# Performance work log

Measured on AMD Instinct MI355X. Metric: run time of the kernel, lower is better.

Reference implementation:

```python
import jax, jax.numpy as jnp
import numpy as np

B, P, T = 128, 196, 20
VOCAB, ENC, EMB, DEC, ATTN = 10000, 2048, 512, 512, 512


def _linear_params(key, out_dim, in_dim):
    kw, kb = jax.random.split(key)
    s = 1.0 / np.sqrt(in_dim)
    W = jax.random.uniform(kw, (out_dim, in_dim), minval=-s, maxval=s, dtype=jnp.float32)
    b = jax.random.uniform(kb, (out_dim,), minval=-s, maxval=s, dtype=jnp.float32)
    return W, b


def setup_inputs() -> dict:
    key = jax.random.key(0)
    ks = jax.random.split(key, 12)
    enc_w, enc_b = _linear_params(ks[0], ATTN, ENC)
    dec_w, dec_b = _linear_params(ks[1], ATTN, DEC)
    full_w, full_b = _linear_params(ks[2], 1, ATTN)
    W_ih, b_ih = _linear_params(ks[3], 4 * DEC, EMB + ENC)
    W_hh, b_hh = _linear_params(ks[4], 4 * DEC, DEC)
    ih_w, ih_b = _linear_params(ks[5], DEC, ENC)
    ic_w, ic_b = _linear_params(ks[6], DEC, ENC)
    fc_w, fc_b = _linear_params(ks[7], VOCAB, DEC)
    return {
        "encoder_out": jax.random.normal(ks[8], (B, P, ENC), dtype=jnp.float32),
        "captions": jax.random.randint(ks[9], (B, T), 0, VOCAB, dtype=jnp.int32),
        "lengths": jax.random.randint(ks[10], (B,), 1, T + 1, dtype=jnp.int32),
        "embedding": jax.random.normal(ks[11], (VOCAB, EMB), dtype=jnp.float32),
        "enc_attn_w": enc_w, "enc_attn_b": enc_b,
        "dec_attn_w": dec_w, "dec_attn_b": dec_b,
        "full_attn_w": full_w, "full_attn_b": full_b,
        "W_ih": W_ih, "b_ih": b_ih, "W_hh": W_hh, "b_hh": b_hh,
        "init_h_w": ih_w, "init_h_b": ih_b,
        "init_c_w": ic_w, "init_c_b": ic_b,
        "fc_w": fc_w, "fc_b": fc_b,
    }


def reference(encoder_out, captions, lengths, embedding,
              enc_attn_w, enc_attn_b, dec_attn_w, dec_attn_b,
              full_attn_w, full_attn_b, W_ih, b_ih, W_hh, b_hh,
              init_h_w, init_h_b, init_c_w, init_c_b, fc_w, fc_b):
    # init hidden state from mean-pooled encoder features
    mean_enc = encoder_out.mean(axis=1)                      # [B, ENC]
    h = mean_enc @ init_h_w.T + init_h_b                      # [B, DEC]
    c = mean_enc @ init_c_w.T + init_c_b

    # loop-invariant encoder projection for additive attention
    attn_enc = jnp.einsum('bpe,ae->bpa', encoder_out, enc_attn_w) + enc_attn_b  # [B, P, ATTN]

    embs = embedding[captions]                                # [B, T, EMB]
    embs_t = jnp.swapaxes(embs, 0, 1)                         # [T, B, EMB]

    dec = h.shape[1]

    def step(carry, emb_t):
        h, c = carry
        # additive attention
        attn_dec = h @ dec_attn_w.T + dec_attn_b              # [B, ATTN]
        energy = jnp.einsum('bpa,a->bp', jax.nn.relu(attn_enc + attn_dec[:, None, :]), full_attn_w[0]) + full_attn_b[0]
        alpha = jax.nn.softmax(energy, axis=1)                # [B, P]
        context = jnp.einsum('bpe,bp->be', encoder_out, alpha)  # [B, ENC]
        # LSTMCell
        x = jnp.concatenate([emb_t, context], axis=1)
        gates = x @ W_ih.T + b_ih + h @ W_hh.T + b_hh          # [B, 4*DEC]
        i, f, g, o = jnp.split(gates, 4, axis=1)
        c_new = jax.nn.sigmoid(f) * c + jax.nn.sigmoid(i) * jnp.tanh(g)
        h_new = jax.nn.sigmoid(o) * jnp.tanh(c_new)
        preds = h_new @ fc_w.T + fc_b                          # [B, VOCAB] (dropout in eval mode = identity)
        return (h_new, c_new), (preds, alpha)

    (_, _), (outputs_t, alphas_t) = jax.lax.scan(step, (h, c), embs_t)
    outputs = jnp.swapaxes(outputs_t, 0, 1)                   # [B, T, VOCAB]
    alphas = jnp.swapaxes(alphas_t, 0, 1)                     # [B, T, P]
    return outputs, alphas
```

## Files before the change

### kernel.cpp

```cpp
#include <hip/hip_runtime.h>

constexpr int kB = 128, kP = 196, kT = 20;
constexpr int kVocab = 10000, kEnc = 2048, kEmb = 512, kDec = 512, kAttn = 512;

typedef __bf16 b16x8 __attribute__((ext_vector_type(8)));
typedef __bf16 b16x4 __attribute__((ext_vector_type(4)));
typedef float f32x4 __attribute__((ext_vector_type(4)));
typedef unsigned short u16x4 __attribute__((ext_vector_type(4)));

__device__ __forceinline__ unsigned short f2bf(float f) {
  unsigned int u = __float_as_uint(f);
  u += 0x7fffu + ((u >> 16) & 1u);
  return (unsigned short)(u >> 16);
}
__device__ __forceinline__ float bf2f(unsigned short h) {
  return __uint_as_float(((unsigned int)h) << 16);
}

__device__ __forceinline__ void async16(const void* g, void* l) {
  __builtin_amdgcn_global_load_lds(
      (const __attribute__((address_space(1))) unsigned int*)g,
      (__attribute__((address_space(3))) unsigned int*)l, 16, 0, 0);
}

template <bool OUT_BF16>
__global__ __launch_bounds__(256) void gemm128(
    const unsigned short* __restrict__ A, const unsigned short* __restrict__ W,
    const float* __restrict__ bias, float* __restrict__ C,
    unsigned short* __restrict__ Cb, int M, int N, int K, long ldc) {
  __shared__ unsigned short sA[128 * 32];
  __shared__ unsigned short sB[128 * 32];
  const int tid = threadIdx.x;
  const int lane = tid & 63;
  const int wave = tid >> 6;
  const int wm = wave >> 1, wn = wave & 1;
  const int m0 = blockIdx.y * 128;
  const int n0 = blockIdx.x * 128;
  const int q = lane >> 4, l = lane & 15;

  const int srow = tid >> 2;
  const int skk = (tid & 3) * 8;
  f32x4 acc[4][4] = {};

  for (int k0 = 0; k0 < K; k0 += 32) {
#pragma unroll
    for (int g = 0; g < 2; g++) {
      const int r = g * 64 + srow;
      async16(A + (long)(m0 + r) * K + k0 + skk, &sA[r * 32 + skk]);
      async16(W + (long)(n0 + r) * K + k0 + skk, &sB[r * 32 + skk]);
    }
    __syncthreads();
    b16x8 af[4], bf[4];
#pragma unroll
    for (int i = 0; i < 4; i++) {
      af[i] = *(const b16x8*)&sA[(wm * 64 + 16 * i + l) * 32 + q * 8];
      bf[i] = *(const b16x8*)&sB[(wn * 64 + 16 * i + l) * 32 + q * 8];
    }
#pragma unroll
    for (int i = 0; i < 4; i++)
#pragma unroll
      for (int j = 0; j < 4; j++)
        acc[i][j] = __builtin_amdgcn_mfma_f32_16x16x32_bf16(af[i], bf[j], acc[i][j], 0, 0, 0);
    __syncthreads();
  }

#pragma unroll
  for (int i = 0; i < 4; i++)
#pragma unroll
    for (int j = 0; j < 4; j++) {
      const int col = n0 + wn * 64 + 16 * j + l;
      const float bv = bias ? bias[col] : 0.0f;
#pragma unroll
      for (int r = 0; r < 4; r++) {
        const int row = m0 + wm * 64 + 16 * i + q * 4 + r;
        const float v = acc[i][j][r] + bv;
        if (OUT_BF16) Cb[(long)row * ldc + col] = f2bf(v);
        else          C[(long)row * ldc + col] = v;
      }
    }
}

template <bool A_BF16, bool OUT_BF16>
__global__ __launch_bounds__(256) void gemm_bt(
    const void* __restrict__ A_, const unsigned short* __restrict__ W,
    const float* __restrict__ bias, float* __restrict__ C,
    unsigned short* __restrict__ Cb, int M, int N, int K, long ldc) {
  const int lane = threadIdx.x & 63;
  const int wave = threadIdx.x >> 6;
  const int wm = wave >> 1, wn = wave & 1;
  const int m0 = blockIdx.y * 64 + wm * 32;
  const int n0 = blockIdx.x * 64 + wn * 32;
  const int q = lane >> 4;
  const int l = lane & 15;
  f32x4 acc[2][2] = {};
  const unsigned short* Ab = (const unsigned short*)A_;
  const float* Af = (const float*)A_;

  for (int k0 = 0; k0 < K; k0 += 32) {
    const int ka = k0 + q * 8;
    b16x8 af[2], wf[2];
#pragma unroll
    for (int i = 0; i < 2; i++) {
      int r = m0 + 16 * i + l;
      if (r >= M) r = M - 1;
      if (A_BF16) {
        af[i] = *(const b16x8*)(Ab + (long)r * K + ka);
      } else {
        const float* p = Af + (long)r * K + ka;
        const f32x4 lo = *(const f32x4*)p;
        const f32x4 hi = *(const f32x4*)(p + 4);
        b16x8 t;
#pragma unroll
        for (int j = 0; j < 4; j++) {
          ((unsigned short*)&t)[j] = f2bf(lo[j]);
          ((unsigned short*)&t)[4 + j] = f2bf(hi[j]);
        }
        af[i] = t;
      }
    }
#pragma unroll
    for (int j = 0; j < 2; j++) {
      int r = n0 + 16 * j + l;
      if (r >= N) r = N - 1;
      wf[j] = *(const b16x8*)(W + (long)r * K + ka);
    }
#pragma unroll
    for (int i = 0; i < 2; i++)
#pragma unroll
      for (int j = 0; j < 2; j++)
        acc[i][j] = __builtin_amdgcn_mfma_f32_16x16x32_bf16(af[i], wf[j], acc[i][j], 0, 0, 0);
  }

#pragma unroll
  for (int i = 0; i < 2; i++)
#pragma unroll
    for (int j = 0; j < 2; j++) {
      const int col = n0 + 16 * j + l;
      if (col >= N) continue;
      const float bv = bias ? bias[col] : 0.0f;
#pragma unroll
      for (int r = 0; r < 4; r++) {
        const int row = m0 + 16 * i + q * 4 + r;
        if (row >= M) continue;
        const float v = acc[i][j][r] + bv;
        if (OUT_BF16) Cb[(long)row * ldc + col] = f2bf(v);
        else          C[(long)row * ldc + col] = v;
      }
    }
}

template <bool SRC_BF16>
__global__ __launch_bounds__(256) void attn_step(
    const void* __restrict__ enc_, const unsigned short* __restrict__ attn_enc_bf,
    const unsigned short* __restrict__ h_bf, const unsigned short* __restrict__ daw_bf,
    const float* __restrict__ dab, const float* __restrict__ faw, const float* __restrict__ fab,
    float* __restrict__ alphas, unsigned short* __restrict__ ctx, int t) {
  const int b = blockIdx.x;
  const int half = blockIdx.y;
  const int tid = threadIdx.x;
  const int lane = tid & 63, wave = tid >> 6;
  __shared__ float h_s[512];
  __shared__ float ad_s[512];
  __shared__ float e_sm[kP];
  __shared__ float red[4];

  h_s[tid] = bf2f(h_bf[b * kDec + tid]);
  h_s[tid + 256] = bf2f(h_bf[b * kDec + tid + 256]);
  __syncthreads();

#pragma unroll
  for (int cc = 0; cc < 2; cc++) {
    const int j = tid + cc * 256;
    float s = dab[j];
    const unsigned short* wrow = daw_bf + (long)j * kDec;
    for (int k = 0; k < kDec; k += 8) {
      const b16x8 wv = *(const b16x8*)(wrow + k);
#pragma unroll
      for (int jj = 0; jj < 8; jj++)
        s += bf2f(((const unsigned short*)&wv)[jj]) * h_s[k + jj];
    }
    ad_s[j] = s;
  }
  __syncthreads();

  float ad8[8], w8[8];
  const int a0 = lane * 8;
#pragma unroll
  for (int j = 0; j < 8; j++) { ad8[j] = ad_s[a0 + j]; w8[j] = faw[a0 + j]; }
  const float fb0 = fab[0];
  for (int p = wave; p < kP; p += 4) {
    const b16x8 rv = *(const b16x8*)(attn_enc_bf + ((long)(b * kP + p)) * kAttn + a0);
    float s = 0.f;
#pragma unroll
    for (int j = 0; j < 8; j++)
      s += w8[j] * fmaxf(bf2f(((const unsigned short*)&rv)[j]) + ad8[j], 0.f);
#pragma unroll
    for (int off = 32; off > 0; off >>= 1) s += __shfl_down(s, off, 64);
    if (lane == 0) e_sm[p] = s + fb0;
  }
  __syncthreads();

  const float v = (tid < kP) ? e_sm[tid] : -3.0e38f;
  float m = v;
#pragma unroll
  for (int off = 32; off > 0; off >>= 1) m = fmaxf(m, __shfl_down(m, off, 64));
  if (lane == 0) red[wave] = m;
  __syncthreads();
  m = fmaxf(fmaxf(red[0], red[1]), fmaxf(red[2], red[3]));
  const float ex = (tid < kP) ? expf(v - m) : 0.f;
  float s = ex;
#pragma unroll
  for (int off = 32; off > 0; off >>= 1) s += __shfl_down(s, off, 64);
  if (lane == 0) red[wave] = s;
  __syncthreads();
  s = red[0] + red[1] + red[2] + red[3];
  __syncthreads();
  const float alpha = ex / s;
  if (tid < kP) {
    e_sm[tid] = alpha;
    if (half == 0) alphas[((long)b * kT + t) * kP + tid] = alpha;
  }
  __syncthreads();

  const int e = half * 1024 + tid * 4;
  float a4[4] = {};
  if (SRC_BF16) {
    const unsigned short* base = (const unsigned short*)enc_ + (long)b * kP * kEnc + e;
    for (int p = 0; p < kP; p++) {
      const float a = e_sm[p];
      const b16x4 rv = *(const b16x4*)(base + (long)p * kEnc);
#pragma unroll
      for (int j = 0; j < 4; j++) a4[j] += a * bf2f(((const unsigned short*)&rv)[j]);
    }
  } else {
    const float* base = (const float*)enc_ + (long)b * kP * kEnc + e;
    for (int p = 0; p < kP; p++) {
      const float a = e_sm[p];
      const f32x4 rv = *(const f32x4*)(base + (long)p * kEnc);
#pragma unroll
      for (int j = 0; j < 4; j++) a4[j] += a * rv[j];
    }
  }
  u16x4 o;
#pragma unroll
  for (int j = 0; j < 4; j++) o[j] = f2bf(a4[j]);
  *(u16x4*)(ctx + (long)b * kEnc + e) = o;
}

__global__ __launch_bounds__(256) void gemm_gates(
    const unsigned short* __restrict__ embs_t, const unsigned short* __restrict__ ctx,
    const unsigned short* __restrict__ hbf, const unsigned short* __restrict__ Wih,
    const unsigned short* __restrict__ Whh, float* __restrict__ gates_part) {
  const int lane = threadIdx.x & 63;
  const int wave = threadIdx.x >> 6;
  const int wm = wave >> 1, wn = wave & 1;
  const int m0 = blockIdx.y * 64 + wm * 32;
  const int n0 = blockIdx.x * 64 + wn * 32;
  const int z = blockIdx.z;
  const int q = lane >> 4;
  const int l = lane & 15;
  f32x4 acc[2][2] = {};
  float* gout = gates_part + (long)z * kB * 2048;

  const int kbeg = z * 768, kend = kbeg + 768;
  for (int k0 = kbeg; k0 < kend; k0 += 32) {
    b16x8 af[2], wf[2];
#pragma unroll
    for (int i = 0; i < 2; i++) {
      const int r = m0 + 16 * i + l;
      const unsigned short* p;
      if (k0 < 512)        p = embs_t + (long)r * kEmb + k0;
      else if (k0 < 2560)  p = ctx + (long)r * kEnc + (k0 - 512);
      else                 p = hbf + (long)r * kDec + (k0 - 2560);
      af[i] = *(const b16x8*)(p + q * 8);
    }
#pragma unroll
    for (int j = 0; j < 2; j++) {
      const int r = n0 + 16 * j + l;
      const unsigned short* p;
      if (k0 < 2560) p = Wih + (long)r * 2560 + k0;
      else           p = Whh + (long)r * 512 + (k0 - 2560);
      wf[j] = *(const b16x8*)(p + q * 8);
    }
#pragma unroll
    for (int i = 0; i < 2; i++)
#pragma unroll
      for (int j = 0; j < 2; j++)
        acc[i][j] = __builtin_amdgcn_mfma_f32_16x16x32_bf16(af[i], wf[j], acc[i][j], 0, 0, 0);
  }
#pragma unroll
  for (int i = 0; i < 2; i++)
#pragma unroll
    for (int j = 0; j < 2; j++) {
      const int col = n0 + 16 * j + l;
#pragma unroll
      for (int r = 0; r < 4; r++) {
        const int row = m0 + 16 * i + q * 4 + r;
        gout[(long)row * 2048 + col] = acc[i][j][r];
      }
    }
}

__global__ __launch_bounds__(256) void lstm_pw(
    const float* __restrict__ gp, const float* __restrict__ bsum,
    float* __restrict__ c, float* __restrict__ h, unsigned short* __restrict__ hbf) {
  const int idx = blockIdx.x * 256 + threadIdx.x;
  const int b = idx >> 9, d = idx & 511;
  float g4[4];
#pragma unroll
  for (int g = 0; g < 4; g++) {
    const int col = g * 512 + d;
    float s = bsum[col];
#pragma unroll
    for (int z = 0; z < 4; z++) s += gp[(long)z * kB * 2048 + (long)b * 2048 + col];
    g4[g] = s;
  }
  const float si = 1.f / (1.f + expf(-g4[0]));
  const float sf = 1.f / (1.f + expf(-g4[1]));
  const float so = 1.f / (1.f + expf(-g4[3]));
  const float cn = sf * c[idx] + si * tanhf(g4[2]);
  const float hn = so * tanhf(cn);
  c[idx] = cn;
  h[idx] = hn;
  hbf[idx] = f2bf(hn);
}

template <bool SRC_BF16>
__global__ __launch_bounds__(256) void mean_kernel(
    const void* __restrict__ enc_, unsigned short* __restrict__ mean_bf) {
  const int b = blockIdx.x;
  const int e = threadIdx.x * 8;
  float acc[8] = {};
  if (SRC_BF16) {
    const unsigned short* base = (const unsigned short*)enc_ + (long)b * kP * kEnc + e;
    for (int p = 0; p < kP; p++) {
      const b16x8 v = *(const b16x8*)(base + (long)p * kEnc);
#pragma unroll
      for (int j = 0; j < 8; j++) acc[j] += bf2f(((const unsigned short*)&v)[j]);
    }
  } else {
    const float* base = (const float*)enc_ + (long)b * kP * kEnc + e;
    for (int p = 0; p < kP; p++) {
      const f32x4 lo = *(const f32x4*)(base + (long)p * kEnc);
      const f32x4 hi = *(const f32x4*)(base + (long)p * kEnc + 4);
#pragma unroll
      for (int j = 0; j < 4; j++) { acc[j] += lo[j]; acc[4 + j] += hi[j]; }
    }
  }
#pragma unroll
  for (int j = 0; j < 8; j++)
    mean_bf[(long)b * kEnc + e + j] = f2bf(acc[j] * (1.0f / 196.0f));
}

__global__ __launch_bounds__(256) void f32_to_bf16_vec(
    const float* __restrict__ src, unsigned short* __restrict__ dst, long n4) {
  for (long i = blockIdx.x * (long)blockDim.x + threadIdx.x; i < n4;
       i += (long)gridDim.x * blockDim.x) {
    const f32x4 v = *(const f32x4*)(src + i * 4);
    u16x4 o;
#pragma unroll
    for (int j = 0; j < 4; j++) o[j] = f2bf(v[j]);
    *(u16x4*)(dst + i * 4) = o;
  }
}

__global__ __launch_bounds__(256) void gather_emb(
    const float* __restrict__ embedding, const int* __restrict__ captions,
    unsigned short* __restrict__ embs) {
  const int r = blockIdx.x;
  const int t = r >> 7, b = r & 127;
  const int cap = captions[b * kT + t];
  const float* src = embedding + (long)cap * kEmb;
  unsigned short* dst = embs + (long)r * kEmb;
  for (int i = threadIdx.x; i < kEmb; i += 256) dst[i] = f2bf(src[i]);
}

__global__ void bias_sum_k(const float* __restrict__ b1, const float* __restrict__ b2,
                           float* __restrict__ o) {
  const int i = blockIdx.x * 256 + threadIdx.x;
  if (i < 2048) o[i] = b1[i] + b2[i];
}

extern "C" void kernel_launch(void* const* d_in, const int* in_sizes, int n_in,
                              void* d_out, int out_size, void* d_ws, size_t ws_size,
                              hipStream_t stream) {
  const float* enc = (const float*)d_in[0];
  const int* captions = (const int*)d_in[1];
  const float* embedding = (const float*)d_in[3];
  const float* eaw = (const float*)d_in[4];
  const float* eab = (const float*)d_in[5];
  const float* daw = (const float*)d_in[6];
  const float* dab = (const float*)d_in[7];
  const float* faw = (const float*)d_in[8];
  const float* fab = (const float*)d_in[9];
  const float* Wih = (const float*)d_in[10];
  const float* bih = (const float*)d_in[11];
  const float* Whh = (const float*)d_in[12];
  const float* bhh = (const float*)d_in[13];
  const float* ihw = (const float*)d_in[14];
  const float* ihb = (const float*)d_in[15];
  const float* icw = (const float*)d_in[16];
  const float* icb = (const float*)d_in[17];
  const float* fcw = (const float*)d_in[18];
  const float* fcb = (const float*)d_in[19];

  float* out = (float*)d_out;
  float* alphas = out + (long)kB * kT * kVocab;

  char* ws = (char*)d_ws;
  size_t off = 0;
  auto alloc = [&](size_t bytes) -> void* {
    void* p = ws + off;
    off = (off + bytes + 255) & ~(size_t)255;
    return p;
  };
  unsigned short* attn_enc_bf = (unsigned short*)alloc((size_t)kB * kP * kAttn * 2);
  unsigned short* Wih_bf = (unsigned short*)alloc((size_t)2048 * 2560 * 2);
  unsigned short* Whh_bf = (unsigned short*)alloc((size_t)2048 * 512 * 2);
  unsigned short* fcw_bf = (unsigned short*)alloc((size_t)kVocab * kDec * 2);
  unsigned short* eaw_bf = (unsigned short*)alloc((size_t)kAttn * kEnc * 2);
  unsigned short* daw_bf = (unsigned short*)alloc((size_t)kAttn * kDec * 2);
  unsigned short* ihw_bf = (unsigned short*)alloc((size_t)kDec * kEnc * 2);
  unsigned short* icw_bf = (unsigned short*)alloc((size_t)kDec * kEnc * 2);
  unsigned short* embs_bf = (unsigned short*)alloc((size_t)kT * kB * kEmb * 2);
  unsigned short* mean_bf = (unsigned short*)alloc((size_t)kB * kEnc * 2);
  float* h = (float*)alloc((size_t)kB * kDec * 4);
  float* c = (float*)alloc((size_t)kB * kDec * 4);
  unsigned short* h_bf = (unsigned short*)alloc((size_t)kB * kDec * 2);
  unsigned short* ctx_bf = (unsigned short*)alloc((size_t)kB * kEnc * 2);
  float* gates_part = (float*)alloc((size_t)4 * kB * 2048 * 4);
  float* bsum = (float*)alloc((size_t)2048 * 4);
  unsigned short* enc_bf = (unsigned short*)alloc((size_t)kB * kP * kEnc * 2);
  const bool have_enc_bf = (off <= ws_size);

  auto cvt = [&](const float* s, unsigned short* d, long n) {
    const long n4 = n / 4;
    long g = (n4 + 255) / 256;
    if (g > 2048) g = 2048;
    f32_to_bf16_vec<<<dim3((unsigned)g), dim3(256), 0, stream>>>(s, d, n4);
  };

  cvt(eaw, eaw_bf, (long)kAttn * kEnc);
  cvt(daw, daw_bf, (long)kAttn * kDec);
  cvt(Wih, Wih_bf, (long)2048 * 2560);
  cvt(Whh, Whh_bf, (long)2048 * 512);
  cvt(fcw, fcw_bf, (long)kVocab * kDec);
  cvt(ihw, ihw_bf, (long)kDec * kEnc);
  cvt(icw, icw_bf, (long)kDec * kEnc);
  if (have_enc_bf) cvt(enc, enc_bf, (long)kB * kP * kEnc);
  bias_sum_k<<<8, 256, 0, stream>>>(bih, bhh, bsum);
  gather_emb<<<kT * kB, 256, 0, stream>>>(embedding, captions, embs_bf);
  if (have_enc_bf)
    mean_kernel<true><<<kB, 256, 0, stream>>>(enc_bf, mean_bf);
  else
    mean_kernel<false><<<kB, 256, 0, stream>>>(enc, mean_bf);

  gemm_bt<true, false><<<dim3(kDec / 64, kB / 64), 256, 0, stream>>>(
      mean_bf, ihw_bf, ihb, h, (unsigned short*)nullptr, kB, kDec, kEnc, kDec);
  gemm_bt<true, false><<<dim3(kDec / 64, kB / 64), 256, 0, stream>>>(
      mean_bf, icw_bf, icb, c, (unsigned short*)nullptr, kB, kDec, kEnc, kDec);
  cvt(h, h_bf, (long)kB * kDec);

  if (have_enc_bf)
    gemm128<true><<<dim3(kAttn / 128, (kB * kP) / 128), 256, 0, stream>>>(
        enc_bf, eaw_bf, eab, (float*)nullptr, attn_enc_bf, kB * kP, kAttn, kEnc, kAttn);
  else
    gemm_bt<false, true><<<dim3(kAttn / 64, (kB * kP) / 64), 256, 0, stream>>>(
        enc, eaw_bf, eab, (float*)nullptr, attn_enc_bf, kB * kP, kAttn, kEnc, kAttn);

  for (int t = 0; t < kT; t++) {
    if (have_enc_bf)
      attn_step<true><<<dim3(kB, 2), 256, 0, stream>>>(
          enc_bf, attn_enc_bf, h_bf, daw_bf, dab, faw, fab, alphas, ctx_bf, t);
    else
      attn_step<false><<<dim3(kB, 2), 256, 0, stream>>>(
          enc, attn_enc_bf, h_bf, daw_bf, dab, faw, fab, alphas, ctx_bf, t);

    gemm_gates<<<dim3(2048 / 64, kB / 64, 4), 256, 0, stream>>>(
        embs_bf + (long)t * kB * kEmb, ctx_bf, h_bf, Wih_bf, Whh_bf, gates_part);

    lstm_pw<<<(kB * kDec) / 256, 256, 0, stream>>>(gates_part, bsum, c, h, h_bf);

    gemm_bt<true, false><<<dim3((kVocab + 63) / 64, kB / 64), 256, 0, stream>>>(
        h_bf, fcw_bf, fcb, out + (long)t * kVocab, (unsigned short*)nullptr,
        kB, kVocab, kDec, (long)kT * kVocab);
  }
}
```

Measured before the change: 2.523 ms.

## Batch decoder attention projection with previous-step FC into one MFMA kernel

```diff
diff --git a/kernel.cpp b/kernel.cpp
--- a/kernel.cpp
+++ b/kernel.cpp
@@ -23,59 +23,48 @@
       (__attribute__((address_space(3))) unsigned int*)l, 16, 0, 0);
 }
 
-template <bool OUT_BF16>
-__global__ __launch_bounds__(256) void gemm128(
+__global__ __launch_bounds__(256) void gemm_ae(
     const unsigned short* __restrict__ A, const unsigned short* __restrict__ W,
-    const float* __restrict__ bias, float* __restrict__ C,
-    unsigned short* __restrict__ Cb, int M, int N, int K, long ldc) {
+    const float* __restrict__ bias, unsigned short* __restrict__ Cb, int M, int K) {
   __shared__ unsigned short sA[128 * 32];
-  __shared__ unsigned short sB[128 * 32];
   const int tid = threadIdx.x;
-  const int lane = tid & 63;
-  const int wave = tid >> 6;
-  const int wm = wave >> 1, wn = wave & 1;
+  const int lane = tid & 63, wave = tid >> 6;
   const int m0 = blockIdx.y * 128;
-  const int n0 = blockIdx.x * 128;
+  const int n0 = blockIdx.x * 64;
   const int q = lane >> 4, l = lane & 15;
-
-  const int srow = tid >> 2;
-  const int skk = (tid & 3) * 8;
-  f32x4 acc[4][4] = {};
+  const int ch0 = tid >> 7, row0 = tid & 127;
+  f32x4 acc[2][4] = {};
 
   for (int k0 = 0; k0 < K; k0 += 32) {
-#pragma unroll
-    for (int g = 0; g < 2; g++) {
-      const int r = g * 64 + srow;
-      async16(A + (long)(m0 + r) * K + k0 + skk, &sA[r * 32 + skk]);
-      async16(W + (long)(n0 + r) * K + k0 + skk, &sB[r * 32 + skk]);
-    }
+    async16(A + (long)(m0 + row0) * K + k0 + ch0 * 8, &sA[(ch0 * 128 + row0) * 8]);
+    async16(A + (long)(m0 + row0) * K + k0 + (ch0 + 2) * 8, &sA[((ch0 + 2) * 128 + row0) * 8]);
+    b16x8 bf4[4];
+#pragma unroll
+    for (int j = 0; j < 4; j++)
+      bf4[j] = *(const b16x8*)(W + (long)(n0 + 16 * j + l) * K + k0 + q * 8);
     __syncthreads();
-    b16x8 af[4], bf[4];
-#pragma unroll
-    for (int i = 0; i < 4; i++) {
-      af[i] = *(const b16x8*)&sA[(wm * 64 + 16 * i + l) * 32 + q * 8];
-      bf[i] = *(const b16x8*)&sB[(wn * 64 + 16 * i + l) * 32 + q * 8];
-    }
-#pragma unroll
-    for (int i = 0; i < 4; i++)
+    b16x8 af[2];
+#pragma unroll
+    for (int i = 0; i < 2; i++)
+      af[i] = *(const b16x8*)&sA[(q * 128 + wave * 32 + 16 * i + l) * 8];
+#pragma unroll
+    for (int i = 0; i < 2; i++)
 #pragma unroll
       for (int j = 0; j < 4; j++)
-        acc[i][j] = __builtin_amdgcn_mfma_f32_16x16x32_bf16(af[i], bf[j], acc[i][j], 0, 0, 0);
+        acc[i][j] = __builtin_amdgcn_mfma_f32_16x16x32_bf16(af[i], bf4[j], acc[i][j], 0, 0, 0);
     __syncthreads();
   }
 
 #pragma unroll
-  for (int i = 0; i < 4; i++)
+  for (int i = 0; i < 2; i++)
 #pragma unroll
     for (int j = 0; j < 4; j++) {
-      const int col = n0 + wn * 64 + 16 * j + l;
-      const float bv = bias ? bias[col] : 0.0f;
+      const int col = n0 + 16 * j + l;
+      const float bv = bias[col];
 #pragma unroll
       for (int r = 0; r < 4; r++) {
-        const int row = m0 + wm * 64 + 16 * i + q * 4 + r;
-        const float v = acc[i][j][r] + bv;
-        if (OUT_BF16) Cb[(long)row * ldc + col] = f2bf(v);
-        else          C[(long)row * ldc + col] = v;
+        const int row = m0 + wave * 32 + 16 * i + q * 4 + r;
+        Cb[(long)row * 512 + col] = f2bf(acc[i][j][r] + bv);
       }
     }
 }
@@ -149,38 +138,89 @@
     }
 }
 
+__global__ __launch_bounds__(256) void adfc_kernel(
+    const unsigned short* __restrict__ h_bf,
+    const unsigned short* __restrict__ daw, const float* __restrict__ dab,
+    float* __restrict__ ad_out,
+    const unsigned short* __restrict__ fcw, const float* __restrict__ fcb,
+    float* __restrict__ preds, long pred_ld) {
+  const int blk = blockIdx.x;
+  const unsigned short* W;
+  const float* bias;
+  float* out;
+  long ldc;
+  int N, m0, n0;
+  if (blk < 16) {
+    if (!ad_out) return;
+    W = daw; bias = dab; out = ad_out; ldc = 512; N = 512;
+    n0 = (blk & 7) * 64; m0 = (blk >> 3) * 64;
+  } else {
+    if (!preds) return;
+    const int idx = blk - 16;
+    W = fcw; bias = fcb; out = preds; ldc = pred_ld; N = kVocab;
+    n0 = (idx % 157) * 64; m0 = (idx / 157) * 64;
+  }
+  const int lane = threadIdx.x & 63, wave = threadIdx.x >> 6;
+  const int wm = wave >> 1, wn = wave & 1;
+  const int q = lane >> 4, l = lane & 15;
+  const int mi = m0 + wm * 32, ni = n0 + wn * 32;
+  f32x4 acc[2][2] = {};
+
+  for (int k0 = 0; k0 < 512; k0 += 64) {
+    b16x8 af[2][2], wf[2][2];
+#pragma unroll
+    for (int u = 0; u < 2; u++) {
+      const int ka = k0 + u * 32 + q * 8;
+#pragma unroll
+      for (int i = 0; i < 2; i++)
+        af[u][i] = *(const b16x8*)(h_bf + (long)(mi + 16 * i + l) * 512 + ka);
+#pragma unroll
+      for (int j = 0; j < 2; j++) {
+        int r = ni + 16 * j + l;
+        if (r >= N) r = N - 1;
+        wf[u][j] = *(const b16x8*)(W + (long)r * 512 + ka);
+      }
+    }
+#pragma unroll
+    for (int u = 0; u < 2; u++)
+#pragma unroll
+      for (int i = 0; i < 2; i++)
+#pragma unroll
+        for (int j = 0; j < 2; j++)
+          acc[i][j] = __builtin_amdgcn_mfma_f32_16x16x32_bf16(af[u][i], wf[u][j], acc[i][j], 0, 0, 0);
+  }
+#pragma unroll
+  for (int i = 0; i < 2; i++)
+#pragma unroll
+    for (int j = 0; j < 2; j++) {
+      const int col = ni + 16 * j + l;
+      if (col >= N) continue;
+      const float bv = bias[col];
+#pragma unroll
+      for (int r = 0; r < 4; r++) {
+        const int row = mi + 16 * i + q * 4 + r;
+        out[(long)row * ldc + col] = acc[i][j][r] + bv;
+      }
+    }
+}
+
 template <bool SRC_BF16>
-__global__ __launch_bounds__(256) void attn_step(
+__global__ __launch_bounds__(256) void attn2(
     const void* __restrict__ enc_, const unsigned short* __restrict__ attn_enc_bf,
-    const unsigned short* __restrict__ h_bf, const unsigned short* __restrict__ daw_bf,
-    const float* __restrict__ dab, const float* __restrict__ faw, const float* __restrict__ fab,
-    float* __restrict__ alphas, unsigned short* __restrict__ ctx, int t) {
+    const float* __restrict__ ad_g, const float* __restrict__ faw,
+    const float* __restrict__ fab, float* __restrict__ alphas,
+    unsigned short* __restrict__ ctx, int t) {
   const int b = blockIdx.x;
   const int half = blockIdx.y;
   const int tid = threadIdx.x;
   const int lane = tid & 63, wave = tid >> 6;
-  __shared__ float h_s[512];
   __shared__ float ad_s[512];
   __shared__ float e_sm[kP];
   __shared__ float red[4];
-
-  h_s[tid] = bf2f(h_bf[b * kDec + tid]);
-  h_s[tid + 256] = bf2f(h_bf[b * kDec + tid + 256]);
-  __syncthreads();
-
-#pragma unroll
-  for (int cc = 0; cc < 2; cc++) {
-    const int j = tid + cc * 256;
-    float s = dab[j];
-    const unsigned short* wrow = daw_bf + (long)j * kDec;
-    for (int k = 0; k < kDec; k += 8) {
-      const b16x8 wv = *(const b16x8*)(wrow + k);
-#pragma unroll
-      for (int jj = 0; jj < 8; jj++)
-        s += bf2f(((const unsigned short*)&wv)[jj]) * h_s[k + jj];
-    }
-    ad_s[j] = s;
-  }
+  __shared__ float cred[128][8];
+
+  ad_s[tid] = ad_g[b * kAttn + tid];
+  ad_s[tid + 256] = ad_g[b * kAttn + tid + 256];
   __syncthreads();
 
   float ad8[8], w8[8];
@@ -222,29 +262,46 @@
   }
   __syncthreads();
 
-  const int e = half * 1024 + tid * 4;
-  float a4[4] = {};
+  const int pg = tid >> 7, th = tid & 127;
+  const int e = half * 1024 + th * 8;
+  float a8[8] = {};
   if (SRC_BF16) {
     const unsigned short* base = (const unsigned short*)enc_ + (long)b * kP * kEnc + e;
-    for (int p = 0; p < kP; p++) {
+    const int pbeg = pg * 98;
+#pragma unroll 2
+    for (int p = pbeg; p < pbeg + 98; p++) {
       const float a = e_sm[p];
-      const b16x4 rv = *(const b16x4*)(base + (long)p * kEnc);
-#pragma unroll
-      for (int j = 0; j < 4; j++) a4[j] += a * bf2f(((const unsigned short*)&rv)[j]);
+      const b16x8 rv = *(const b16x8*)(base + (long)p * kEnc);
+#pragma unroll
+      for (int j = 0; j < 8; j++) a8[j] += a * bf2f(((const unsigned short*)&rv)[j]);
     }
   } else {
     const float* base = (const float*)enc_ + (long)b * kP * kEnc + e;
-    for (int p = 0; p < kP; p++) {
+    const int pbeg = pg * 98;
+#pragma unroll 2
+    for (int p = pbeg; p < pbeg + 98; p++) {
       const float a = e_sm[p];
-      const f32x4 rv = *(const f32x4*)(base + (long)p * kEnc);
-#pragma unroll
-      for (int j = 0; j < 4; j++) a4[j] += a * rv[j];
-    }
-  }
-  u16x4 o;
-#pragma unroll
-  for (int j = 0; j < 4; j++) o[j] = f2bf(a4[j]);
-  *(u16x4*)(ctx + (long)b * kEnc + e) = o;
+      const f32x4 lo = *(const f32x4*)(base + (long)p * kEnc);
+      const f32x4 hi = *(const f32x4*)(base + (long)p * kEnc + 4);
+#pragma unroll
+      for (int j = 0; j < 4; j++) { a8[j] += a * lo[j]; a8[4 + j] += a * hi[j]; }
+    }
+  }
+  if (pg == 1) {
+#pragma unroll
+    for (int j = 0; j < 8; j++) cred[th][j] = a8[j];
+  }
+  __syncthreads();
+  if (pg == 0) {
+    u16x4 o0, o1;
+#pragma unroll
+    for (int j = 0; j < 4; j++) {
+      o0[j] = f2bf(a8[j] + cred[th][j]);
+      o1[j] = f2bf(a8[4 + j] + cred[th][4 + j]);
+    }
+    *(u16x4*)(ctx + (long)b * kEnc + e) = o0;
+    *(u16x4*)(ctx + (long)b * kEnc + e + 4) = o1;
+  }
 }
 
 __global__ __launch_bounds__(256) void gemm_gates(
@@ -427,6 +484,7 @@
   float* h = (float*)alloc((size_t)kB * kDec * 4);
   float* c = (float*)alloc((size_t)kB * kDec * 4);
   unsigned short* h_bf = (unsigned short*)alloc((size_t)kB * kDec * 2);
+  float* ad_buf = (float*)alloc((size_t)kB * kAttn * 4);
   unsigned short* ctx_bf = (unsigned short*)alloc((size_t)kB * kEnc * 2);
   float* gates_part = (float*)alloc((size_t)4 * kB * 2048 * 4);
   float* bsum = (float*)alloc((size_t)2048 * 4);
@@ -462,27 +520,30 @@
   cvt(h, h_bf, (long)kB * kDec);
 
   if (have_enc_bf)
-    gemm128<true><<<dim3(kAttn / 128, (kB * kP) / 128), 256, 0, stream>>>(
-        enc_bf, eaw_bf, eab, (float*)nullptr, attn_enc_bf, kB * kP, kAttn, kEnc, kAttn);
+    gemm_ae<<<dim3(kAttn / 64, (kB * kP) / 128), 256, 0, stream>>>(
+        enc_bf, eaw_bf, eab, attn_enc_bf, kB * kP, kEnc);
   else
     gemm_bt<false, true><<<dim3(kAttn / 64, (kB * kP) / 64), 256, 0, stream>>>(
         enc, eaw_bf, eab, (float*)nullptr, attn_enc_bf, kB * kP, kAttn, kEnc, kAttn);
 
   for (int t = 0; t < kT; t++) {
+    adfc_kernel<<<330, 256, 0, stream>>>(
+        h_bf, daw_bf, dab, ad_buf, fcw_bf, fcb,
+        (t == 0) ? (float*)nullptr : out + (long)(t - 1) * kVocab, (long)kT * kVocab);
+
     if (have_enc_bf)
-      attn_step<true><<<dim3(kB, 2), 256, 0, stream>>>(
-          enc_bf, attn_enc_bf, h_bf, daw_bf, dab, faw, fab, alphas, ctx_bf, t);
+      attn2<true><<<dim3(kB, 2), 256, 0, stream>>>(
+          enc_bf, attn_enc_bf, ad_buf, faw, fab, alphas, ctx_bf, t);
     else
-      attn_step<false><<<dim3(kB, 2), 256, 0, stream>>>(
-          enc, attn_enc_bf, h_bf, daw_bf, dab, faw, fab, alphas, ctx_bf, t);
+      attn2<false><<<dim3(kB, 2), 256, 0, stream>>>(
+          enc, attn_enc_bf, ad_buf, faw, fab, alphas, ctx_bf, t);
 
     gemm_gates<<<dim3(2048 / 64, kB / 64, 4), 256, 0, stream>>>(
         embs_bf + (long)t * kB * kEmb, ctx_bf, h_bf, Wih_bf, Whh_bf, gates_part);
 
     lstm_pw<<<(kB * kDec) / 256, 256, 0, stream>>>(gates_part, bsum, c, h, h_bf);
-
-    gemm_bt<true, false><<<dim3((kVocab + 63) / 64, kB / 64), 256, 0, stream>>>(
-        h_bf, fcw_bf, fcb, out + (long)t * kVocab, (unsigned short*)nullptr,
-        kB, kVocab, kDec, (long)kT * kVocab);
-  }
-}
+  }
+  adfc_kernel<<<330, 256, 0, stream>>>(
+      h_bf, daw_bf, dab, (float*)nullptr, fcw_bf, fcb,
+      out + (long)19 * kVocab, (long)kT * kVocab);
+}
```

Result: faster. 2.449 ms (-2.9%).
